# Performance work log

Hardware: AMD Instinct MI355X
Metric: run time of the kernel (lower is better)

The kernel has to match this reference:

```python
import jax, jax.numpy as jnp
import numpy as np

EPS = 1e-5
NEG_SLOPE = 0.1


def conv2d(x, w, b, pad):
    y = jax.lax.conv_general_dilated(x, w, (1, 1), ((pad[0], pad[0]), (pad[1], pad[1])),
                                     dimension_numbers=('NCHW', 'OIHW', 'NCHW'))
    return y + b[None, :, None, None]


def bn(x, g, b, m, v):
    # inference-mode BatchNorm2d
    scale = g / jnp.sqrt(v + EPS)
    return (x - m[None, :, None, None]) * scale[None, :, None, None] + b[None, :, None, None]


def leaky(x):
    return jnp.where(x >= 0, x, NEG_SLOPE * x)


def pos_embed(C, T, V):
    # STTFormer-style sinusoidal embedding over joint index, repeated per frame
    pos = jnp.tile(jnp.arange(V, dtype=jnp.float32), T)[:, None]            # (T*V, 1)
    div = jnp.exp(jnp.arange(0, C, 2, dtype=jnp.float32) * (-np.log(10000.0) / C))
    pe = jnp.zeros((T * V, C), jnp.float32)
    pe = pe.at[:, 0::2].set(jnp.sin(pos * div)).at[:, 1::2].set(jnp.cos(pos * div))
    return pe.reshape(T, V, C).transpose(2, 0, 1)[None]                      # (1, C, T, V)


def ema(x, c1w, c1b, c3w, c3b, gng, gnb, groups):
    # Efficient Multi-scale Attention (EMA) module
    b, c, h, w = x.shape
    cg = c // groups
    gx = x.reshape(b * groups, cg, h, w)
    x_h = gx.mean(axis=3, keepdims=True)                                     # (bg, cg, h, 1)
    x_w = jnp.swapaxes(gx.mean(axis=2, keepdims=True), 2, 3)                 # (bg, cg, w, 1)
    hw = conv2d(jnp.concatenate([x_h, x_w], axis=2), c1w, c1b, (0, 0))       # 1x1 conv
    xh, xw = hw[:, :, :h], hw[:, :, h:]
    g = gx * jax.nn.sigmoid(xh) * jax.nn.sigmoid(jnp.swapaxes(xw, 2, 3))
    # GroupNorm(cg, cg): one channel per group -> per-channel spatial norm
    mu = g.mean((2, 3), keepdims=True)
    var = g.var((2, 3), keepdims=True)
    x1 = (g - mu) / jnp.sqrt(var + EPS) * gng[None, :, None, None] + gnb[None, :, None, None]
    x2 = conv2d(gx, c3w, c3b, (1, 1))                                        # 3x3 conv
    x11 = jax.nn.softmax(x1.mean((2, 3))[:, None, :], axis=-1)               # (bg, 1, cg)
    x21 = jax.nn.softmax(x2.mean((2, 3))[:, None, :], axis=-1)
    x12 = x2.reshape(b * groups, cg, h * w)
    x22 = x1.reshape(b * groups, cg, h * w)
    weights = (x11 @ x12 + x21 @ x22).reshape(b * groups, 1, h, w)
    return (gx * jax.nn.sigmoid(weights)).reshape(b, c, h, w)


def _forward(x, atten_weight, qkv_w, qkv_b, alphas, att0s, nets_w, nets_b,
             bn1_g, bn1_b, bn1_m, bn1_v,
             e1_c1w, e1_c1b, e1_c3w, e1_c3b, e1_gng, e1_gnb,
             bn2_g, bn2_b, bn2_m, bn2_v,
             nett_w, nett_b, bn3_g, bn3_b, bn3_m, bn3_v,
             e2_c1w, e2_c1b, e2_c3w, e2_c3b, e2_gng, e2_gnb,
             bn4_g, bn4_b, bn4_m, bn4_v):
    N, C, T, V = x.shape
    H = alphas.shape[1]
    D = qkv_w.shape[0] // (2 * H)
    xs = pos_embed(C, T, V) + x
    # 1x1 conv to q,k
    qk = jnp.einsum('oc,nctv->notv', qkv_w, xs) + qkv_b[None, :, None, None]
    qk = qk.reshape(N, 2 * H, D, T, V)
    q, k = qk[:, :H], qk[:, H:]
    # tanh attention over joints (V x V), scaled, weighted, plus learned bias table
    att = jnp.tanh(jnp.einsum('nhctu,nhctv->nhuv', q, k) / (D * T)) * alphas
    att = att * atten_weight[None, None] + att0s
    xs = jnp.einsum('nctu,nhuv->nhctv', x, att).reshape(N, H * C, T, V)
    x_ress = x  # in_channels == out_channels -> identity residual
    xs = leaky(bn(conv2d(xs, nets_w, nets_b, (0, 1)), bn1_g, bn1_b, bn1_m, bn1_v) + x_ress)
    xs = leaky(bn(ema(xs, e1_c1w, e1_c1b, e1_c3w, e1_c3b, e1_gng, e1_gnb, 16),
                  bn2_g, bn2_b, bn2_m, bn2_v) + x_ress)
    xt = leaky(bn(conv2d(xs, nett_w, nett_b, (2, 0)), bn3_g, bn3_b, bn3_m, bn3_v) + xs)
    xt = leaky(bn(ema(xt, e2_c1w, e2_c1b, e2_c3w, e2_c3b, e2_gng, e2_gnb, 32),
                  bn4_g, bn4_b, bn4_m, bn4_v) + xs)
    return xt


def setup_inputs() -> dict:
    key = jax.random.key(0)
    N, C, T, V, H, D, O = 64, 64, 120, 25, 3, 64, 64
    cg1, cg2 = O // 16, O // 32
    ks = jax.random.split(key, 16)
    f32 = jnp.float32

    def bn_params(k, c):
        k1, k2 = jax.random.split(k)
        return (jnp.ones(c, f32), jnp.zeros(c, f32),
                jax.random.normal(k1, (c,), f32) * 0.1,
                jax.random.uniform(k2, (c,), f32) + 0.5)

    bn1 = bn_params(ks[5], O)
    bn2 = bn_params(ks[6], O)
    bn3 = bn_params(ks[7], O)
    bn4 = bn_params(ks[8], O)
    return {
        'x': jax.random.normal(ks[0], (N, C, T, V), f32),
        'atten_weight': jax.random.uniform(ks[1], (V, V), f32),
        'qkv_w': jax.random.normal(ks[2], (2 * H * D, C), f32) * 0.05,
        'qkv_b': jnp.zeros(2 * H * D, f32),
        'alphas': jnp.ones((1, H, 1, 1), f32),
        'att0s': jnp.ones((1, H, V, V), f32) / V,
        'nets_w': jax.random.normal(ks[3], (O, C * H, 1, 3), f32) * 0.05,
        'nets_b': jnp.zeros(O, f32),
        'bn1_g': bn1[0], 'bn1_b': bn1[1], 'bn1_m': bn1[2], 'bn1_v': bn1[3],
        'e1_c1w': jax.random.normal(ks[9], (cg1, cg1, 1, 1), f32) * 0.1,
        'e1_c1b': jnp.zeros(cg1, f32),
        'e1_c3w': jax.random.normal(ks[10], (cg1, cg1, 3, 3), f32) * 0.1,
        'e1_c3b': jnp.zeros(cg1, f32),
        'e1_gng': jnp.ones(cg1, f32), 'e1_gnb': jnp.zeros(cg1, f32),
        'bn2_g': bn2[0], 'bn2_b': bn2[1], 'bn2_m': bn2[2], 'bn2_v': bn2[3],
        'nett_w': jax.random.normal(ks[4], (O, O, 5, 1), f32) * 0.05,
        'nett_b': jnp.zeros(O, f32),
        'bn3_g': bn3[0], 'bn3_b': bn3[1], 'bn3_m': bn3[2], 'bn3_v': bn3[3],
        'e2_c1w': jax.random.normal(ks[11], (cg2, cg2, 1, 1), f32) * 0.1,
        'e2_c1b': jnp.zeros(cg2, f32),
        'e2_c3w': jax.random.normal(ks[12], (cg2, cg2, 3, 3), f32) * 0.1,
        'e2_c3b': jnp.zeros(cg2, f32),
        'e2_gng': jnp.ones(cg2, f32), 'e2_gnb': jnp.zeros(cg2, f32),
        'bn4_g': bn4[0], 'bn4_b': bn4[1], 'bn4_m': bn4[2], 'bn4_v': bn4[3],
    }


def reference(x, atten_weight, qkv_w, qkv_b, alphas, att0s, nets_w, nets_b,
              bn1_g, bn1_b, bn1_m, bn1_v,
              e1_c1w, e1_c1b, e1_c3w, e1_c3b, e1_gng, e1_gnb,
              bn2_g, bn2_b, bn2_m, bn2_v,
              nett_w, nett_b, bn3_g, bn3_b, bn3_m, bn3_v,
              e2_c1w, e2_c1b, e2_c3w, e2_c3b, e2_gng, e2_gnb,
              bn4_g, bn4_b, bn4_m, bn4_v):
    return _forward(x, atten_weight, qkv_w, qkv_b, alphas, att0s, nets_w, nets_b,
                    bn1_g, bn1_b, bn1_m, bn1_v,
                    e1_c1w, e1_c1b, e1_c3w, e1_c3b, e1_gng, e1_gnb,
                    bn2_g, bn2_b, bn2_m, bn2_v,
                    nett_w, nett_b, bn3_g, bn3_b, bn3_m, bn3_v,
                    e2_c1w, e2_c1b, e2_c3w, e2_c3b, e2_gng, e2_gnb,
                    bn4_g, bn4_b, bn4_m, bn4_v)
```

## Files before the change

kernel.cpp:

```cpp
#include <hip/hip_runtime.h>

typedef float v2f __attribute__((ext_vector_type(2)));
__device__ __forceinline__ v2f mk2(float a, float b){ v2f r; r.x=a; r.y=b; return r; }
__device__ __forceinline__ v2f bc2(float x){ v2f r; r.x=x; r.y=x; return r; }

__device__ __forceinline__ float sigm(float x){ return 1.f/(1.f+__expf(-x)); }

__device__ __forceinline__ float waveReduceSum(float v){
  #pragma unroll
  for (int o = 32; o > 0; o >>= 1) v += __shfl_down(v, o, 64);
  return v;
}
__device__ __forceinline__ float blockReduceSum(float v, float* red4, int tid){
  v = waveReduceSum(v);
  __syncthreads();
  if ((tid & 63) == 0) red4[tid >> 6] = v;
  __syncthreads();
  return red4[0] + red4[1] + red4[2] + red4[3];
}

__global__ __launch_bounds__(256) void zeroS_kernel(float* __restrict__ S){
  int i = blockIdx.x*256 + threadIdx.x;
  if (i < 120000) S[i] = 0.f;
}

__global__ __launch_bounds__(256) void att_partial_kernel(
    const float* __restrict__ x, const float* __restrict__ qkv_w, const float* __restrict__ qkv_b,
    float* __restrict__ S)
{
  const int nh = blockIdx.x;
  const int tc = blockIdx.y;
  const int n = nh / 3, h = nh % 3;
  const int tid = threadIdx.x;
  __shared__ float Wq[4096], Wk[4096];
  __shared__ float xt[1600];
  __shared__ float Qs[1600], Ks[1600];
  __shared__ float qb[64], kb[64];
  for (int i = tid; i < 4096; i += 256){
    int cq = i & 63, c = i >> 6;
    Wq[c*64+cq] = qkv_w[(size_t)(h*64 + cq)*64 + c];
    Wk[c*64+cq] = qkv_w[(size_t)((3+h)*64 + cq)*64 + c];
  }
  if (tid < 64){ qb[tid] = qkv_b[h*64 + tid]; kb[tid] = qkv_b[(3+h)*64 + tid]; }
  float pe_reg[7]; int goff[7];
  #pragma unroll
  for (int k=0;k<7;k++){
    int i = tid + k*256;
    if (i < 1600){
      int c = i/25, uu = i%25;
      float freq = __expf(-(float)(2*(c>>1)) * 0.14391156835f);
      float a = (float)uu * freq;
      pe_reg[k] = (c & 1) ? cosf(a) : sinf(a);
      goff[k] = (n*64 + c)*3000 + uu;
    }
  }
  v2f saccv[2] = { {0.f,0.f}, {0.f,0.f} };
  float sacc4 = 0.f;
  const int u = tid / 5, v0 = (tid % 5) * 5;
  for (int t = tc*15; t < tc*15 + 15; ++t){
    __syncthreads();
    #pragma unroll
    for (int k=0;k<7;k++){
      int i = tid + k*256;
      if (i < 1600) xt[i] = x[goff[k] + t*25] + pe_reg[k];
    }
    __syncthreads();
    if (tid < 160){
      int qk = tid / 80; int r = tid % 80; int cq0 = (r/5)*4; int u0 = (r%5)*5;
      const float* W = qk ? Wk : Wq;
      const float* bb = qk ? kb : qb;
      v2f accv[2][5];
      #pragma unroll
      for (int p=0;p<2;p++){
        v2f b = mk2(bb[cq0+2*p], bb[cq0+2*p+1]);
        #pragma unroll
        for (int j=0;j<5;j++) accv[p][j] = b;
      }
      const float* Wb = &W[cq0];
      const float* xb = &xt[u0];
      #pragma unroll 8
      for (int c = 0; c < 64; ++c){
        float xv[5];
        #pragma unroll
        for (int j=0;j<5;j++) xv[j] = xb[c*25 + j];
        v2f w0 = mk2(Wb[c*64+0], Wb[c*64+1]);
        v2f w1 = mk2(Wb[c*64+2], Wb[c*64+3]);
        #pragma unroll
        for (int j=0;j<5;j++){
          accv[0][j] += w0 * bc2(xv[j]);
          accv[1][j] += w1 * bc2(xv[j]);
        }
      }
      float* Out = qk ? Ks : Qs;
      #pragma unroll
      for (int p=0;p<2;p++)
        #pragma unroll
        for (int j=0;j<5;j++){
          Out[(cq0+2*p)*25 + u0 + j]   = accv[p][j].x;
          Out[(cq0+2*p+1)*25 + u0 + j] = accv[p][j].y;
        }
    }
    __syncthreads();
    if (tid < 125){
      const float* Qb = &Qs[u];
      const float* Kb = &Ks[v0];
      #pragma unroll 8
      for (int c = 0; c < 64; ++c){
        float q = Qb[c*25];
        saccv[0] += bc2(q) * mk2(Kb[c*25+0], Kb[c*25+1]);
        saccv[1] += bc2(q) * mk2(Kb[c*25+2], Kb[c*25+3]);
        sacc4 += q * Kb[c*25+4];
      }
    }
  }
  if (tid < 125){
    float* dst = S + (size_t)nh*625 + u*25 + v0;
    atomicAdd(dst + 0, saccv[0].x);
    atomicAdd(dst + 1, saccv[0].y);
    atomicAdd(dst + 2, saccv[1].x);
    atomicAdd(dst + 3, saccv[1].y);
    atomicAdd(dst + 4, sacc4);
  }
}

__global__ __launch_bounds__(256) void att_finalize_kernel(
    float* __restrict__ S, const float* __restrict__ attw,
    const float* __restrict__ alphas, const float* __restrict__ att0s)
{
  int idx = blockIdx.x*256 + threadIdx.x;
  if (idx >= 120000) return;
  int nh = idx / 625, uv = idx % 625;
  int h = nh % 3;
  float a = tanhf(S[idx] * (1.f/7680.f)) * alphas[h];
  S[idx] = a * attw[uv] + att0s[h*625 + uv];
}

__global__ __launch_bounds__(256,4) void stage1_kernel(
    const float* __restrict__ x, const float* __restrict__ att,
    const float* __restrict__ nets_w, const float* __restrict__ nets_b,
    const float* __restrict__ bng, const float* __restrict__ bnb,
    const float* __restrict__ bnm, const float* __restrict__ bnv,
    float* __restrict__ s1)
{
  __shared__ float smem[7872];
  float* sc    = smem;
  float* sh    = smem + 64;
  float* att_s = smem + 128;
  float* xts   = smem + 2003;
  float* xbp   = smem + 5267;
  const int n = blockIdx.x, t0 = blockIdx.y*2;
  const int tid = threadIdx.x;

  for (int i=tid;i<1875;i+=256) att_s[i] = att[(size_t)n*1875 + i];
  for (int i=tid;i<3200;i+=256){
    int c=i/50, r=i%50;
    xts[c*51 + r] = x[((size_t)(n*64+c)*120 + t0 + r/25)*25 + (r%25)];
  }
  if (tid < 192){
    int row=tid>>2, p=tid&3;
    xbp[row*54 + ((p&1)?26:0) + ((p>>1)?27:0)] = 0.f;
  }
  if (tid < 64){
    float s = bng[tid]*rsqrtf(bnv[tid]+1e-5f);
    sc[tid]=s; sh[tid]=bnb[tid]-bnm[tid]*s;
  }
  __syncthreads();

  const int op = tid>>3, r = tid&7, tt = r>>2, vq = r&3;
  const int o0 = op*2, v0q = vq*7, nv = (vq<3)?7:4;
  v2f accv[7];
  #pragma unroll
  for (int j=0;j<7;j++) accv[j] = bc2(0.f);

  for (int q=0; q<4; ++q){
    const int hc0 = q*48;
    if (tid < 240){
      int hcH = tid % 48, vg = tid / 48;
      int hc = hc0 + hcH;
      int h = hc>>6, c = hc&63, v0 = vg*5;
      v2f av[5];
      #pragma unroll
      for (int j=0;j<5;j++) av[j] = bc2(0.f);
      const float* xr0 = &xts[c*51];
      for (int u=0;u<25;u++){
        v2f xv = mk2(xr0[u], xr0[u+25]);
        const float* ap = &att_s[(h*25+u)*25 + v0];
        #pragma unroll
        for (int j=0;j<5;j++) av[j] += bc2(ap[j]) * xv;
      }
      #pragma unroll
      for (int j=0;j<5;j++){
        xbp[hcH*54 + 1 + v0 + j]  = av[j].x;
        xbp[hcH*54 + 28 + v0 + j] = av[j].y;
      }
    }
    __syncthreads();

    const float* xbase = &xbp[tt*27 + v0q];
    const float* wg0 = nets_w + (size_t)o0*576 + hc0*3;
    const float* wg1 = wg0 + 576;
    #pragma unroll 4
    for (int hcL=0; hcL<48; ++hcL){
      float xr[9];
      #pragma unroll
      for (int j=0;j<9;j++) xr[j] = xbase[hcL*54 + j];
      v2f w0 = mk2(wg0[hcL*3+0], wg1[hcL*3+0]);
      v2f w1 = mk2(wg0[hcL*3+1], wg1[hcL*3+1]);
      v2f w2 = mk2(wg0[hcL*3+2], wg1[hcL*3+2]);
      #pragma unroll
      for (int j=0;j<7;j++)
        accv[j] += w0*bc2(xr[j]) + w1*bc2(xr[j+1]) + w2*bc2(xr[j+2]);
    }
    __syncthreads();
  }

  float b0 = nets_b[o0], b1 = nets_b[o0+1];
  const int t = t0 + tt;
  #pragma unroll
  for (int j=0;j<7;j++){
    if (j < nv){
      int v = v0q + j;
      size_t base0 = ((size_t)(n*64+o0)*120 + t)*25 + v;
      size_t base1 = ((size_t)(n*64+o0+1)*120 + t)*25 + v;
      float y0 = (accv[j].x + b0)*sc[o0]   + sh[o0]   + x[base0];
      float y1 = (accv[j].y + b1)*sc[o0+1] + sh[o0+1] + x[base1];
      y0 = (y0>=0.f)? y0 : 0.1f*y0;
      y1 = (y1>=0.f)? y1 : 0.1f*y1;
      s1[base0] = y0;
      s1[base1] = y1;
    }
  }
}

__global__ __launch_bounds__(256) void stage3_kernel(
    const float* __restrict__ s2, const float* __restrict__ nett_w, const float* __restrict__ nett_b,
    const float* __restrict__ bng, const float* __restrict__ bnb,
    const float* __restrict__ bnm, const float* __restrict__ bnv,
    float* __restrict__ s3)
{
  const int n = blockIdx.x, t0 = blockIdx.y*4;
  const int tid = threadIdx.x;
  __shared__ float tile[12800];
  __shared__ float sc[64], sh[64];
  for (int i=tid;i<12800;i+=256){
    int c=i/200, r=i%200, tt=r/25, v=r%25;
    int t = t0 + tt - 2;
    tile[i] = (t>=0 && t<120) ? s2[((size_t)(n*64+c)*120 + t)*25 + v] : 0.f;
  }
  if (tid < 64){
    float s = bng[tid]*rsqrtf(bnv[tid]+1e-5f);
    sc[tid]=s; sh[tid]=bnb[tid]-bnm[tid]*s;
  }
  __syncthreads();
  for (int task=tid; task<800; task+=256){
    int og = task/25, v = task%25; int o0 = og*2;
    v2f accv[4];
    { v2f b = mk2(nett_b[o0], nett_b[o0+1]);
      #pragma unroll
      for (int k=0;k<4;k++) accv[k]=b; }
    const float* tb = &tile[v];
    const float* wbase = nett_w + (size_t)o0*320;
    #pragma unroll 4
    for (int c=0;c<64;c++){
      float xr[8];
      #pragma unroll
      for (int k=0;k<8;k++) xr[k] = tb[c*200 + k*25];
      v2f w[5];
      #pragma unroll
      for (int d=0;d<5;d++) w[d] = mk2(wbase[c*5 + d], wbase[320 + c*5 + d]);
      #pragma unroll
      for (int k=0;k<4;k++){
        #pragma unroll
        for (int d=0;d<5;d++) accv[k] += w[d]*bc2(xr[k+d]);
      }
    }
    #pragma unroll
    for (int k=0;k<4;k++){
      int t=t0+k;
      float r0 = tile[o0*200     + (k+2)*25 + v];
      float r1 = tile[(o0+1)*200 + (k+2)*25 + v];
      float y0 = accv[k].x*sc[o0]   + sh[o0]   + r0;
      float y1 = accv[k].y*sc[o0+1] + sh[o0+1] + r1;
      y0 = (y0>=0.f)? y0 : 0.1f*y0;
      y1 = (y1>=0.f)? y1 : 0.1f*y1;
      s3[((size_t)(n*64+o0)*120   + t)*25 + v] = y0;
      s3[((size_t)(n*64+o0+1)*120 + t)*25 + v] = y1;
    }
  }
}

template<int CG, int G>
__global__ __launch_bounds__(256) void ema_kernel(
    const float* __restrict__ in, const float* __restrict__ res,
    const float* __restrict__ c1w, const float* __restrict__ c1b,
    const float* __restrict__ c3w, const float* __restrict__ c3b,
    const float* __restrict__ gng, const float* __restrict__ gnb,
    const float* __restrict__ bng, const float* __restrict__ bnb,
    const float* __restrict__ bnm, const float* __restrict__ bnv,
    float* __restrict__ out)
{
  constexpr int PR = 122*27;
  __shared__ float gx[CG*PR];
  __shared__ float xh[CG*120], xw[CG*25];
  __shared__ float sigh[CG*120], sigw[CG*25];
  __shared__ float red4[4];
  __shared__ float c1w_s[CG*CG], c1b_s[CG], c3w_s[CG*CG*9], c3b_s[CG],
                   gng_s[CG], gnb_s[CG], sc_s[CG], sh_s[CG];
  const int tid = threadIdx.x;
  const int b = blockIdx.x; const int n = b / G; const int grp = b % G; const int c0 = grp*CG;
  const float* src = in + (size_t)(n*64 + c0)*3000;
  for (int i = tid; i < CG*PR; i += 256) gx[i] = 0.f;
  if (tid < CG*CG) c1w_s[tid] = c1w[tid];
  if (tid < CG*CG*9) c3w_s[tid] = c3w[tid];
  if (tid < CG){
    c1b_s[tid] = c1b[tid];
    c3b_s[tid] = c3b[tid]; gng_s[tid]=gng[tid]; gnb_s[tid]=gnb[tid];
    float s = bng[c0+tid] * rsqrtf(bnv[c0+tid]+1e-5f);
    sc_s[tid] = s; sh_s[tid] = bnb[c0+tid] - bnm[c0+tid]*s;
  }
  __syncthreads();
  for (int i = tid; i < CG*3000; i += 256){
    int cc = i/3000, p = i%3000, t = p/25, v = p%25;
    gx[cc*PR + (t+1)*27 + (v+1)] = src[i];
  }
  __syncthreads();
  for (int j = tid; j < CG*120; j += 256){
    int cc=j/120, t=j%120; float s=0;
    for (int v=0;v<25;v++) s += gx[cc*PR+(t+1)*27+(v+1)];
    xh[j] = s*(1.f/25.f);
  }
  for (int j = tid; j < CG*25; j += 256){
    int cc=j/25, v=j%25; float s=0;
    for (int t=0;t<120;t++) s += gx[cc*PR+(t+1)*27+(v+1)];
    xw[j] = s*(1.f/120.f);
  }
  __syncthreads();
  for (int j = tid; j < CG*120; j += 256){
    int cc=j/120, t=j%120; float s=c1b_s[cc];
    #pragma unroll
    for (int i=0;i<CG;i++) s += c1w_s[cc*CG+i]*xh[i*120+t];
    sigh[j] = sigm(s);
  }
  for (int j = tid; j < CG*25; j += 256){
    int cc=j/25, v=j%25; float s=c1b_s[cc];
    #pragma unroll
    for (int i=0;i<CG;i++) s += c1w_s[cc*CG+i]*xw[i*25+v];
    sigw[j] = sigm(s);
  }
  __syncthreads();
  float gs[CG], gss[CG];
  #pragma unroll
  for (int cc=0;cc<CG;cc++){ gs[cc]=0.f; gss[cc]=0.f; }
  for (int p = tid; p < 3000; p += 256){
    int t=p/25, v=p%25;
    #pragma unroll
    for (int cc=0;cc<CG;cc++){
      float g = gx[cc*PR+(t+1)*27+(v+1)]*sigh[cc*120+t]*sigw[cc*25+v];
      gs[cc]+=g; gss[cc]+=g*g;
    }
  }
  #pragma unroll
  for (int cc=0;cc<CG;cc++){
    gs[cc]  = blockReduceSum(gs[cc],  red4, tid);
    gss[cc] = blockReduceSum(gss[cc], red4, tid);
  }
  float mu[CG], inv[CG];
  #pragma unroll
  for (int cc=0;cc<CG;cc++){
    mu[cc] = gs[cc]*(1.f/3000.f);
    float var = gss[cc]*(1.f/3000.f) - mu[cc]*mu[cc];
    inv[cc] = rsqrtf(fmaxf(var, 0.f) + 1e-5f);
  }
  float x11[CG];
  { float mx = gnb_s[0];
    #pragma unroll
    for (int cc=1;cc<CG;cc++) mx = fmaxf(mx, gnb_s[cc]);
    float sum=0;
    #pragma unroll
    for (int cc=0;cc<CG;cc++){ x11[cc]=__expf(gnb_s[cc]-mx); sum+=x11[cc]; }
    float r = 1.f/sum;
    #pragma unroll
    for (int cc=0;cc<CG;cc++) x11[cc]*=r; }
  float Sall[CG];
  #pragma unroll
  for (int i=0;i<CG;i++){ float s=0; for (int t=0;t<120;t++) s += xh[i*120+t]; Sall[i]=s*25.f; }
  float m2[CG];
  #pragma unroll
  for (int cc=0;cc<CG;cc++){
    float acc = c3b_s[cc]*3000.f;
    #pragma unroll
    for (int i=0;i<CG;i++){
      #pragma unroll
      for (int dy=0;dy<3;dy++){
        #pragma unroll
        for (int dx=0;dx<3;dx++){
          float w = c3w_s[(cc*CG+i)*9+dy*3+dx];
          float ss = Sall[i];
          int re = -1, ce = -1;
          if (dy==0){ ss -= 25.f*xh[i*120+119]; re=119; }
          else if (dy==2){ ss -= 25.f*xh[i*120+0]; re=0; }
          if (dx==0){ ss -= 120.f*xw[i*25+24]; ce=24; }
          else if (dx==2){ ss -= 120.f*xw[i*25+0]; ce=0; }
          if (re>=0 && ce>=0) ss += gx[i*PR + (re+1)*27 + (ce+1)];
          acc += w*ss;
        }
      }
    }
    m2[cc] = acc*(1.f/3000.f);
  }
  float x21[CG];
  { float mx = m2[0];
    #pragma unroll
    for (int cc=1;cc<CG;cc++) mx = fmaxf(mx, m2[cc]);
    float sum=0;
    #pragma unroll
    for (int cc=0;cc<CG;cc++){ x21[cc]=__expf(m2[cc]-mx); sum+=x21[cc]; }
    float r = 1.f/sum;
    #pragma unroll
    for (int cc=0;cc<CG;cc++) x21[cc]*=r; }
  float wm[CG*9]; float bm=0.f, kc=0.f;
  #pragma unroll
  for (int k=0;k<CG*9;k++){
    float s=0;
    #pragma unroll
    for (int cc=0;cc<CG;cc++) s += x11[cc]*c3w_s[cc*CG*9 + k];
    wm[k]=s;
  }
  float ga[CG];
  #pragma unroll
  for (int cc=0;cc<CG;cc++){
    bm += x11[cc]*c3b_s[cc];
    ga[cc] = x21[cc]*gng_s[cc]*inv[cc];
    kc += x21[cc]*(gnb_s[cc] - mu[cc]*gng_s[cc]*inv[cc]);
  }
  const float base = bm + kc;
  for (int p = tid; p < 3000; p += 256){
    int t=p/25, v=p%25;
    float wsum = base;
    #pragma unroll
    for (int i=0;i<CG;i++){
      const float* gp = &gx[i*PR + t*27 + v];
      wsum += wm[i*9+0]*gp[0]  + wm[i*9+1]*gp[1]  + wm[i*9+2]*gp[2]
            + wm[i*9+3]*gp[27] + wm[i*9+4]*gp[28] + wm[i*9+5]*gp[29]
            + wm[i*9+6]*gp[54] + wm[i*9+7]*gp[55] + wm[i*9+8]*gp[56];
    }
    #pragma unroll
    for (int cc=0;cc<CG;cc++){
      float g = gx[cc*PR+(t+1)*27+(v+1)]*sigh[cc*120+t]*sigw[cc*25+v];
      wsum += ga[cc]*g;
    }
    float sw = sigm(wsum);
    #pragma unroll
    for (int cc=0;cc<CG;cc++){
      float val = gx[cc*PR+(t+1)*27+(v+1)]*sw;
      float y = val*sc_s[cc] + sh_s[cc] + res[(size_t)(n*64+c0+cc)*3000 + p];
      y = (y >= 0.f) ? y : 0.1f*y;
      out[(size_t)(n*64+c0+cc)*3000 + p] = y;
    }
  }
}

extern "C" void kernel_launch(void* const* d_in, const int* in_sizes, int n_in,
                              void* d_out, int out_size, void* d_ws, size_t ws_size,
                              hipStream_t stream)
{
  const float* x      = (const float*)d_in[0];
  const float* attw   = (const float*)d_in[1];
  const float* qkv_w  = (const float*)d_in[2];
  const float* qkv_b  = (const float*)d_in[3];
  const float* alphas = (const float*)d_in[4];
  const float* att0s  = (const float*)d_in[5];
  const float* nets_w = (const float*)d_in[6];
  const float* nets_b = (const float*)d_in[7];
  const float* bn1g = (const float*)d_in[8];  const float* bn1b = (const float*)d_in[9];
  const float* bn1m = (const float*)d_in[10]; const float* bn1v = (const float*)d_in[11];
  const float* e1c1w = (const float*)d_in[12]; const float* e1c1b = (const float*)d_in[13];
  const float* e1c3w = (const float*)d_in[14]; const float* e1c3b = (const float*)d_in[15];
  const float* e1gng = (const float*)d_in[16]; const float* e1gnb = (const float*)d_in[17];
  const float* bn2g = (const float*)d_in[18]; const float* bn2b = (const float*)d_in[19];
  const float* bn2m = (const float*)d_in[20]; const float* bn2v = (const float*)d_in[21];
  const float* nettw = (const float*)d_in[22]; const float* nettb = (const float*)d_in[23];
  const float* bn3g = (const float*)d_in[24]; const float* bn3b = (const float*)d_in[25];
  const float* bn3m = (const float*)d_in[26]; const float* bn3v = (const float*)d_in[27];
  const float* e2c1w = (const float*)d_in[28]; const float* e2c1b = (const float*)d_in[29];
  const float* e2c3w = (const float*)d_in[30]; const float* e2c3b = (const float*)d_in[31];
  const float* e2gng = (const float*)d_in[32]; const float* e2gnb = (const float*)d_in[33];
  const float* bn4g = (const float*)d_in[34]; const float* bn4b = (const float*)d_in[35];
  const float* bn4m = (const float*)d_in[36]; const float* bn4v = (const float*)d_in[37];

  float* S    = (float*)d_ws;
  float* outf = (float*)d_out;
  float* xbuf = (float*)d_in[0];

  zeroS_kernel<<<469,256,0,stream>>>(S);
  att_partial_kernel<<<dim3(192,8),256,0,stream>>>(x, qkv_w, qkv_b, S);
  att_finalize_kernel<<<469,256,0,stream>>>(S, attw, alphas, att0s);
  stage1_kernel<<<dim3(64,60),256,0,stream>>>(x, S, nets_w, nets_b, bn1g,bn1b,bn1m,bn1v, outf);
  ema_kernel<4,16><<<1024,256,0,stream>>>(outf, x,
      e1c1w,e1c1b,e1c3w,e1c3b,e1gng,e1gnb, bn2g,bn2b,bn2m,bn2v, xbuf);
  stage3_kernel<<<dim3(64,30),256,0,stream>>>(xbuf, nettw, nettb, bn3g,bn3b,bn3m,bn3v, outf);
  ema_kernel<2,32><<<2048,256,0,stream>>>(outf, xbuf,
      e2c1w,e2c1b,e2c3w,e2c3b,e2gng,e2gnb, bn4g,bn4b,bn4m,bn4v, outf);
}
```

Measured before the change: 989.3 us.

## Read QKV weights from global memory and overlap staging with score computation

Drops the shared-memory copies of the Q/K weight matrices and biases, so each thread reads its weight rows straight from global memory (through cache) and holds the bias in registers. This shrinks LDS use per block and adds a launch-bounds occupancy hint. The time loop is also restructured so that staging the next frame's input overlaps with the score accumulation of the current frame, which removes one barrier per iteration. The cost is that weights are now fetched from global or L2 memory inside the inner loop rather than from LDS.

```diff
diff --git a/kernel.cpp b/kernel.cpp
--- a/kernel.cpp
+++ b/kernel.cpp
@@ -24,7 +24,7 @@
   if (i < 120000) S[i] = 0.f;
 }
 
-__global__ __launch_bounds__(256) void att_partial_kernel(
+__global__ __launch_bounds__(256,4) void att_partial_kernel(
     const float* __restrict__ x, const float* __restrict__ qkv_w, const float* __restrict__ qkv_b,
     float* __restrict__ S)
 {
@@ -32,16 +32,9 @@
   const int tc = blockIdx.y;
   const int n = nh / 3, h = nh % 3;
   const int tid = threadIdx.x;
-  __shared__ float Wq[4096], Wk[4096];
   __shared__ float xt[1600];
   __shared__ float Qs[1600], Ks[1600];
-  __shared__ float qb[64], kb[64];
-  for (int i = tid; i < 4096; i += 256){
-    int cq = i & 63, c = i >> 6;
-    Wq[c*64+cq] = qkv_w[(size_t)(h*64 + cq)*64 + c];
-    Wk[c*64+cq] = qkv_w[(size_t)((3+h)*64 + cq)*64 + c];
-  }
-  if (tid < 64){ qb[tid] = qkv_b[h*64 + tid]; kb[tid] = qkv_b[(3+h)*64 + tid]; }
+
   float pe_reg[7]; int goff[7];
   #pragma unroll
   for (int k=0;k<7;k++){
@@ -54,66 +47,79 @@
       goff[k] = (n*64 + c)*3000 + uu;
     }
   }
+
+  const int qk = tid / 80, rr = tid % 80, cq0 = (rr/5)*4, u0 = (rr%5)*5;
+  const float* Wg = qkv_w + (size_t)((qk ? 3+h : h)*64 + cq0)*64;
+  v2f bias0, bias1;
+  { const float* bb = qkv_b + (qk ? 3+h : h)*64 + cq0;
+    bias0 = mk2(bb[0], bb[1]); bias1 = mk2(bb[2], bb[3]); }
+
+  const int u = tid / 5, v0 = (tid % 5) * 5;
   v2f saccv[2] = { {0.f,0.f}, {0.f,0.f} };
   float sacc4 = 0.f;
-  const int u = tid / 5, v0 = (tid % 5) * 5;
-  for (int t = tc*15; t < tc*15 + 15; ++t){
-    __syncthreads();
+
+  auto do_stage = [&](int t){
     #pragma unroll
     for (int k=0;k<7;k++){
       int i = tid + k*256;
       if (i < 1600) xt[i] = x[goff[k] + t*25] + pe_reg[k];
     }
-    __syncthreads();
+  };
+  auto do_qk = [&](){
     if (tid < 160){
-      int qk = tid / 80; int r = tid % 80; int cq0 = (r/5)*4; int u0 = (r%5)*5;
-      const float* W = qk ? Wk : Wq;
-      const float* bb = qk ? kb : qb;
-      v2f accv[2][5];
-      #pragma unroll
-      for (int p=0;p<2;p++){
-        v2f b = mk2(bb[cq0+2*p], bb[cq0+2*p+1]);
-        #pragma unroll
-        for (int j=0;j<5;j++) accv[p][j] = b;
-      }
-      const float* Wb = &W[cq0];
+      v2f a0[5], a1[5];
+      #pragma unroll
+      for (int j=0;j<5;j++){ a0[j]=bias0; a1[j]=bias1; }
       const float* xb = &xt[u0];
       #pragma unroll 8
       for (int c = 0; c < 64; ++c){
         float xv[5];
         #pragma unroll
         for (int j=0;j<5;j++) xv[j] = xb[c*25 + j];
-        v2f w0 = mk2(Wb[c*64+0], Wb[c*64+1]);
-        v2f w1 = mk2(Wb[c*64+2], Wb[c*64+3]);
+        v2f w0 = mk2(Wg[c],     Wg[64+c]);
+        v2f w1 = mk2(Wg[128+c], Wg[192+c]);
         #pragma unroll
         for (int j=0;j<5;j++){
-          accv[0][j] += w0 * bc2(xv[j]);
-          accv[1][j] += w1 * bc2(xv[j]);
+          a0[j] += w0 * bc2(xv[j]);
+          a1[j] += w1 * bc2(xv[j]);
         }
       }
       float* Out = qk ? Ks : Qs;
       #pragma unroll
-      for (int p=0;p<2;p++)
-        #pragma unroll
-        for (int j=0;j<5;j++){
-          Out[(cq0+2*p)*25 + u0 + j]   = accv[p][j].x;
-          Out[(cq0+2*p+1)*25 + u0 + j] = accv[p][j].y;
-        }
-    }
+      for (int j=0;j<5;j++){
+        Out[(cq0+0)*25 + u0 + j] = a0[j].x;
+        Out[(cq0+1)*25 + u0 + j] = a0[j].y;
+        Out[(cq0+2)*25 + u0 + j] = a1[j].x;
+        Out[(cq0+3)*25 + u0 + j] = a1[j].y;
+      }
+    }
+  };
+  auto do_score = [&](){
+    const float* Qb = &Qs[u];
+    const float* Kb = &Ks[v0];
+    #pragma unroll 8
+    for (int c = 0; c < 64; ++c){
+      float q = Qb[c*25];
+      saccv[0] += bc2(q) * mk2(Kb[c*25+0], Kb[c*25+1]);
+      saccv[1] += bc2(q) * mk2(Kb[c*25+2], Kb[c*25+3]);
+      sacc4 += q * Kb[c*25+4];
+    }
+  };
+
+  const int t0 = tc*15;
+  do_stage(t0);
+  __syncthreads();
+  do_qk();
+  __syncthreads();
+  for (int t = t0+1; t < t0+15; ++t){
+    do_stage(t);
+    if (tid < 125) do_score();
     __syncthreads();
-    if (tid < 125){
-      const float* Qb = &Qs[u];
-      const float* Kb = &Ks[v0];
-      #pragma unroll 8
-      for (int c = 0; c < 64; ++c){
-        float q = Qb[c*25];
-        saccv[0] += bc2(q) * mk2(Kb[c*25+0], Kb[c*25+1]);
-        saccv[1] += bc2(q) * mk2(Kb[c*25+2], Kb[c*25+3]);
-        sacc4 += q * Kb[c*25+4];
-      }
-    }
+    do_qk();
+    __syncthreads();
   }
   if (tid < 125){
+    do_score();
     float* dst = S + (size_t)nh*625 + u*25 + v0;
     atomicAdd(dst + 0, saccv[0].x);
     atomicAdd(dst + 1, saccv[0].y);
```

Result: no change. 999.0 us (+1.0%).

## Fold Q and K projections into a precomputed bilinear matrix for attention scores

Applied to the files above, without the earlier changes.

Attention scores Q^T K are rewritten as x^T (Wq^T Wk) x plus bias cross-terms. A new prep kernel computes the 64x64 product matrix, the bias-projected vectors and the constant bias dot product once per head, and stores them in the output buffer as scratch. The partial kernel then does one 64x64 matvec per frame instead of two projections, and uses less shared memory because the two weight matrices and the Q and K buffers are no longer kept. The constant term is added in finalize, scaled by the 120 frames. Work per frame drops, at the cost of an extra small launch and reuse of the output buffer before stage1 overwrites it.

```diff
diff --git a/kernel.cpp b/kernel.cpp
--- a/kernel.cpp
+++ b/kernel.cpp
@@ -24,24 +24,57 @@
   if (i < 120000) S[i] = 0.f;
 }
 
-__global__ __launch_bounds__(256) void att_partial_kernel(
-    const float* __restrict__ x, const float* __restrict__ qkv_w, const float* __restrict__ qkv_b,
-    float* __restrict__ S)
+__global__ __launch_bounds__(256) void att_prep_kernel(
+    const float* __restrict__ qkv_w, const float* __restrict__ qkv_b, float* __restrict__ Mbuf)
+{
+  const int h = blockIdx.x;
+  const int tid = threadIdx.x;
+  __shared__ float Wq[4096], Wk[4096];
+  for (int i=tid;i<4096;i+=256){
+    Wq[i] = qkv_w[(size_t)h*4096 + i];
+    Wk[i] = qkv_w[(size_t)(3+h)*4096 + i];
+  }
+  __syncthreads();
+  int c = tid>>2, cp0 = (tid&3)*16;
+  float acc[16];
+  #pragma unroll
+  for (int j=0;j<16;j++) acc[j]=0.f;
+  for (int cq=0;cq<64;cq++){
+    float wq = Wq[cq*64+c];
+    #pragma unroll
+    for (int j=0;j<16;j++) acc[j] += wq*Wk[cq*64+cp0+j];
+  }
+  float* dst = Mbuf + (size_t)h*4290 + c*65 + cp0;
+  #pragma unroll
+  for (int j=0;j<16;j++) dst[j] = acc[j];
+  if (tid < 128){
+    int row = tid>>6, cp = tid&63;
+    const float* W = row ? Wq : Wk;
+    const float* bvec = qkv_b + (row ? (3+h)*64 : h*64);
+    float s=0;
+    for (int cq=0;cq<64;cq++) s += bvec[cq]*W[cq*64+cp];
+    Mbuf[(size_t)h*4290 + (64+row)*65 + cp] = s;
+  }
+  if (tid==0){
+    const float* qb = qkv_b + h*64; const float* kb = qkv_b + (3+h)*64;
+    float s=0;
+    for (int i=0;i<64;i++) s += qb[i]*kb[i];
+    Mbuf[12870 + h] = s;
+  }
+}
+
+__global__ __launch_bounds__(256,4) void att_partial_kernel(
+    const float* __restrict__ x, const float* __restrict__ Mbuf, float* __restrict__ S)
 {
   const int nh = blockIdx.x;
   const int tc = blockIdx.y;
   const int n = nh / 3, h = nh % 3;
   const int tid = threadIdx.x;
-  __shared__ float Wq[4096], Wk[4096];
   __shared__ float xt[1600];
-  __shared__ float Qs[1600], Ks[1600];
-  __shared__ float qb[64], kb[64];
-  for (int i = tid; i < 4096; i += 256){
-    int cq = i & 63, c = i >> 6;
-    Wq[c*64+cq] = qkv_w[(size_t)(h*64 + cq)*64 + c];
-    Wk[c*64+cq] = qkv_w[(size_t)((3+h)*64 + cq)*64 + c];
-  }
-  if (tid < 64){ qb[tid] = qkv_b[h*64 + tid]; kb[tid] = qkv_b[(3+h)*64 + tid]; }
+  __shared__ float Ybuf[1650];
+  __shared__ float Ms[4290];
+  for (int i=tid;i<4290;i+=256) Ms[i] = Mbuf[(size_t)h*4290 + i];
+
   float pe_reg[7]; int goff[7];
   #pragma unroll
   for (int k=0;k<7;k++){
@@ -57,6 +90,9 @@
   v2f saccv[2] = { {0.f,0.f}, {0.f,0.f} };
   float sacc4 = 0.f;
   const int u = tid / 5, v0 = (tid % 5) * 5;
+  const int yc0 = (tid/25)*8, yv = tid%25;
+  const int xrow = 64 + (tid-200)/25, xv = (tid-200)%25;
+
   for (int t = tc*15; t < tc*15 + 15; ++t){
     __syncthreads();
     #pragma unroll
@@ -65,45 +101,37 @@
       if (i < 1600) xt[i] = x[goff[k] + t*25] + pe_reg[k];
     }
     __syncthreads();
-    if (tid < 160){
-      int qk = tid / 80; int r = tid % 80; int cq0 = (r/5)*4; int u0 = (r%5)*5;
-      const float* W = qk ? Wk : Wq;
-      const float* bb = qk ? kb : qb;
-      v2f accv[2][5];
-      #pragma unroll
-      for (int p=0;p<2;p++){
-        v2f b = mk2(bb[cq0+2*p], bb[cq0+2*p+1]);
-        #pragma unroll
-        for (int j=0;j<5;j++) accv[p][j] = b;
-      }
-      const float* Wb = &W[cq0];
-      const float* xb = &xt[u0];
+    if (tid < 200){
+      v2f a[4];
+      #pragma unroll
+      for (int j=0;j<4;j++) a[j] = bc2(0.f);
+      const float* mb = &Ms[yc0*65];
+      const float* xb = &xt[yv];
       #pragma unroll 8
-      for (int c = 0; c < 64; ++c){
-        float xv[5];
-        #pragma unroll
-        for (int j=0;j<5;j++) xv[j] = xb[c*25 + j];
-        v2f w0 = mk2(Wb[c*64+0], Wb[c*64+1]);
-        v2f w1 = mk2(Wb[c*64+2], Wb[c*64+3]);
-        #pragma unroll
-        for (int j=0;j<5;j++){
-          accv[0][j] += w0 * bc2(xv[j]);
-          accv[1][j] += w1 * bc2(xv[j]);
-        }
-      }
-      float* Out = qk ? Ks : Qs;
-      #pragma unroll
-      for (int p=0;p<2;p++)
-        #pragma unroll
-        for (int j=0;j<5;j++){
-          Out[(cq0+2*p)*25 + u0 + j]   = accv[p][j].x;
-          Out[(cq0+2*p+1)*25 + u0 + j] = accv[p][j].y;
-        }
+      for (int cp=0; cp<64; ++cp){
+        float xvv = xb[cp*25];
+        a[0] += mk2(mb[cp],     mb[cp+65])  * bc2(xvv);
+        a[1] += mk2(mb[cp+130], mb[cp+195]) * bc2(xvv);
+        a[2] += mk2(mb[cp+260], mb[cp+325]) * bc2(xvv);
+        a[3] += mk2(mb[cp+390], mb[cp+455]) * bc2(xvv);
+      }
+      #pragma unroll
+      for (int j=0;j<4;j++){
+        Ybuf[(yc0+2*j)*25 + yv]   = a[j].x;
+        Ybuf[(yc0+2*j+1)*25 + yv] = a[j].y;
+      }
+    } else if (tid < 250){
+      const float* mb = &Ms[xrow*65];
+      const float* xb = &xt[xv];
+      float s = 0.f;
+      #pragma unroll 8
+      for (int cp=0; cp<64; ++cp) s += mb[cp]*xb[cp*25];
+      Ybuf[xrow*25 + xv] = s;
     }
     __syncthreads();
     if (tid < 125){
-      const float* Qb = &Qs[u];
-      const float* Kb = &Ks[v0];
+      const float* Qb = &xt[u];
+      const float* Kb = &Ybuf[v0];
       #pragma unroll 8
       for (int c = 0; c < 64; ++c){
         float q = Qb[c*25];
@@ -111,6 +139,11 @@
         saccv[1] += bc2(q) * mk2(Kb[c*25+2], Kb[c*25+3]);
         sacc4 += q * Kb[c*25+4];
       }
+      float ybu = Ybuf[65*25 + u];
+      const float* av = &Ybuf[64*25 + v0];
+      saccv[0] += mk2(av[0]+ybu, av[1]+ybu);
+      saccv[1] += mk2(av[2]+ybu, av[3]+ybu);
+      sacc4    += av[4]+ybu;
     }
   }
   if (tid < 125){
@@ -125,13 +158,14 @@
 
 __global__ __launch_bounds__(256) void att_finalize_kernel(
     float* __restrict__ S, const float* __restrict__ attw,
-    const float* __restrict__ alphas, const float* __restrict__ att0s)
+    const float* __restrict__ alphas, const float* __restrict__ att0s,
+    const float* __restrict__ c0buf)
 {
   int idx = blockIdx.x*256 + threadIdx.x;
   if (idx >= 120000) return;
   int nh = idx / 625, uv = idx % 625;
   int h = nh % 3;
-  float a = tanhf(S[idx] * (1.f/7680.f)) * alphas[h];
+  float a = tanhf((S[idx] + 120.f*c0buf[h]) * (1.f/7680.f)) * alphas[h];
   S[idx] = a * attw[uv] + att0s[h*625 + uv];
 }
 
@@ -491,10 +525,12 @@
   float* S    = (float*)d_ws;
   float* outf = (float*)d_out;
   float* xbuf = (float*)d_in[0];
-
+  float* Mbuf = (float*)d_out;
+
+  att_prep_kernel<<<3,256,0,stream>>>(qkv_w, qkv_b, Mbuf);
   zeroS_kernel<<<469,256,0,stream>>>(S);
-  att_partial_kernel<<<dim3(192,8),256,0,stream>>>(x, qkv_w, qkv_b, S);
-  att_finalize_kernel<<<469,256,0,stream>>>(S, attw, alphas, att0s);
+  att_partial_kernel<<<dim3(192,8),256,0,stream>>>(x, Mbuf, S);
+  att_finalize_kernel<<<469,256,0,stream>>>(S, attw, alphas, att0s, Mbuf + 12870);
   stage1_kernel<<<dim3(64,60),256,0,stream>>>(x, S, nets_w, nets_b, bn1g,bn1b,bn1m,bn1v, outf);
   ema_kernel<4,16><<<1024,256,0,stream>>>(outf, x,
       e1c1w,e1c1b,e1c3w,e1c3b,e1gng,e1gnb, bn2g,bn2b,bn2m,bn2v, xbuf);
```

Result: slower. 1.066 ms (+7.7%).
